# Kernel tuning notes

Measured on AMD Instinct MI355X. Metric: run time of the kernel, lower is better.

## Reference

```python
import jax, jax.numpy as jnp
import numpy as np

H = 8
DQ = 32
DK = 32
DV = 32
DC = DQ + DK  # concat dim for additive attention


def setup_inputs() -> dict:
    key = jax.random.key(0)
    ks = jax.random.split(key, 8)
    bs, Lq, Lk = 2, 384, 384
    q = jax.random.normal(ks[0], (bs, Lq, H * DQ), jnp.float32)
    k = jax.random.normal(ks[1], (bs, Lk, H * DK), jnp.float32)
    v = jax.random.normal(ks[2], (bs, Lk, H * DV), jnp.float32)
    q_sequence_lengths = jax.random.randint(ks[3], (bs,), 1, Lq + 1, dtype=jnp.int32)
    k_sequence_lengths = jax.random.randint(ks[4], (bs,), 1, Lk + 1, dtype=jnp.int32)
    bound = 1.0 / np.sqrt(DC)
    w1 = jax.random.uniform(ks[5], (H, DC, DC), jnp.float32, -bound, bound)
    b1 = jax.random.uniform(ks[6], (H, DC), jnp.float32, -bound, bound)
    w2 = jax.random.uniform(ks[7], (H, DC), jnp.float32, -1.0, 1.0)
    return {"q": q, "k": k, "v": v,
            "q_sequence_lengths": q_sequence_lengths,
            "k_sequence_lengths": k_sequence_lengths,
            "w1": w1, "b1": b1, "w2": w2}


def reference(q, k, v, q_sequence_lengths, k_sequence_lengths, w1, b1, w2):
    bs, Lq, _ = q.shape
    Lk = k.shape[1]
    # split heads: (b, h, L, d)
    qh = q.reshape(bs, Lq, H, DQ).transpose(0, 2, 1, 3)
    kh = k.reshape(bs, Lk, H, DK).transpose(0, 2, 1, 3)
    vh = v.reshape(bs, Lk, H, DV).transpose(0, 2, 1, 3)
    # additive scores: tanh(cat(q_i, k_j) @ W1 + b1) @ w2
    # cat @ W1 == q @ W1[:DQ] + k @ W1[DQ:]  (avoids materializing the cat)
    qW = jnp.einsum('bhqd,hde->bhqe', qh, w1[:, :DQ, :])
    kW = jnp.einsum('bhkd,hde->bhke', kh, w1[:, DQ:, :])
    hid = jnp.tanh(qW[:, :, :, None, :] + kW[:, :, None, :, :] + b1[None, :, None, None, :])  # (b,h,q,k,DC)
    scores = jnp.einsum('bhqke,he->bhqk', hid, w2)
    # key-side length mask (end padded)
    kmask = jnp.arange(Lk)[None, :] < k_sequence_lengths[:, None]  # (b, Lk)
    scores = jnp.where(kmask[:, None, None, :], scores, jnp.float32(-1e9))
    att = jax.nn.softmax(scores, axis=-1)  # (b,h,q,k)
    out = jnp.einsum('bhqk,bhkd->bqhd', att, vh)  # (b,q,h,DV)
    # query-side length mask zeros out padded query rows
    qmask = jnp.arange(Lq)[None, :] < q_sequence_lengths[:, None]  # (b, Lq)
    out = out * qmask[:, :, None, None].astype(out.dtype)
    return out.reshape(bs, Lq, H * DV), att
```

## Files before the change

### kernel.cpp

```cpp
#include <hip/hip_runtime.h>

#define NH 8
#define LQ 384
#define LK 384
#define BS 2

__global__ __launch_bounds__(256) void pre_ek_kernel(
    const float* __restrict__ kin, const float* __restrict__ w1,
    const float* __restrict__ b1, float* __restrict__ ws)
{
    __shared__ float tile[32][65];
    const int bid = blockIdx.x;
    const int bh = bid / 12, kt = bid % 12;
    const int b = bh >> 3, h = bh & 7;
    const int k0 = kt * 32;
    const int lane = threadIdx.x & 63, w = threadIdx.x >> 6;

    float w1c[32];
    const float* w1p = w1 + (size_t)(h * 64 + 32) * 64 + lane;
    #pragma unroll
    for (int d = 0; d < 32; ++d) w1c[d] = w1p[d * 64];
    const float bv = b1[h * 64 + lane];

    #pragma unroll
    for (int s = 0; s < 8; ++s) {
        int kr = w * 8 + s;
        const float* krow = kin + ((size_t)(b * LK + k0 + kr)) * (NH * 32) + h * 32;
        float acc = bv;
        #pragma unroll
        for (int d = 0; d < 32; ++d) acc = __builtin_fmaf(krow[d], w1c[d], acc);
        tile[kr][lane] = __expf(acc + acc);
    }
    __syncthreads();
    #pragma unroll
    for (int r = 0; r < 2; ++r) {
        int f = threadIdx.x + r * 256;
        int e4 = f >> 5, k32 = f & 31;
        float4 o;
        o.x = tile[k32][e4 * 4 + 0];
        o.y = tile[k32][e4 * 4 + 1];
        o.z = tile[k32][e4 * 4 + 2];
        o.w = tile[k32][e4 * 4 + 3];
        ((float4*)ws)[((size_t)(bh * 16 + e4)) * LK + k0 + k32] = o;
    }
}

__global__ __launch_bounds__(256) void attn_kernel(
    const float* __restrict__ qin, const float* __restrict__ vin,
    const int* __restrict__ qlens, const int* __restrict__ klens,
    const float* __restrict__ w1, const float* __restrict__ w2g,
    const float* __restrict__ ws,
    float* __restrict__ outg, float* __restrict__ attg)
{
    __shared__ __align__(16) float att_s[8][LK];
    __shared__ __align__(16) float eqs[8 * 64];
    __shared__ __align__(16) float w2s[4][64];

    const int tid = threadIdx.x, wave = tid >> 6, lane = tid & 63;
    const int bh = blockIdx.x / 48, tile = blockIdx.x % 48;
    const int b = bh >> 3, h = bh & 7;
    const int q0 = tile * 8;
    const int klen = klens[b], qlen = qlens[b];
    const int r0 = wave * 2;

    {
        const float* w1p = w1 + (size_t)h * 64 * 64 + lane;
        const float* q0p = qin + ((size_t)(b * LQ + q0 + r0)) * (NH * 32) + h * 32;
        const float* q1p = q0p + (NH * 32);
        float a0 = 0.f, a1 = 0.f;
        #pragma unroll
        for (int d = 0; d < 32; ++d) {
            float wv = w1p[d * 64];
            a0 = __builtin_fmaf(q0p[d], wv, a0);
            a1 = __builtin_fmaf(q1p[d], wv, a1);
        }
        eqs[(r0 + 0) * 64 + lane] = __expf(a0 + a0);
        eqs[(r0 + 1) * 64 + lane] = __expf(a1 + a1);
        w2s[wave][lane] = w2g[h * 64 + lane];
    }

    float sc0[6] = {0.f,0.f,0.f,0.f,0.f,0.f};
    float sc1[6] = {0.f,0.f,0.f,0.f,0.f,0.f};
    const float4* ekq  = (const float4*)ws + ((size_t)bh * 16) * LK + lane;
    const float4* eq0p = (const float4*)(eqs + (r0 + 0) * 64);
    const float4* eq1p = (const float4*)(eqs + (r0 + 1) * 64);
    const float4* w2p  = (const float4*)(&w2s[wave][0]);

    #pragma unroll 4
    for (int e4 = 0; e4 < 16; ++e4) {
        float4 e0 = eq0p[e4];
        float4 e1 = eq1p[e4];
        float4 wv = w2p[e4];
        const float4* kp = ekq + e4 * LK;
        #pragma unroll
        for (int c = 0; c < 6; ++c) {
            float4 kv = kp[c * 64];
            {
                float t0 = __builtin_fmaf(e0.x, kv.x, 1.f);
                float t1 = __builtin_fmaf(e0.y, kv.y, 1.f);
                float t2 = __builtin_fmaf(e0.z, kv.z, 1.f);
                float t3 = __builtin_fmaf(e0.w, kv.w, 1.f);
                float p12 = t0 * t1, p34 = t2 * t3;
                float n12 = wv.x * t1; n12 = __builtin_fmaf(wv.y, t0, n12);
                float n34 = wv.z * t3; n34 = __builtin_fmaf(wv.w, t2, n34);
                float num = n12 * p34; num = __builtin_fmaf(n34, p12, num);
                sc0[c] = __builtin_fmaf(num, __builtin_amdgcn_rcpf(p12 * p34), sc0[c]);
            }
            {
                float t0 = __builtin_fmaf(e1.x, kv.x, 1.f);
                float t1 = __builtin_fmaf(e1.y, kv.y, 1.f);
                float t2 = __builtin_fmaf(e1.z, kv.z, 1.f);
                float t3 = __builtin_fmaf(e1.w, kv.w, 1.f);
                float p12 = t0 * t1, p34 = t2 * t3;
                float n12 = wv.x * t1; n12 = __builtin_fmaf(wv.y, t0, n12);
                float n34 = wv.z * t3; n34 = __builtin_fmaf(wv.w, t2, n34);
                float num = n12 * p34; num = __builtin_fmaf(n34, p12, num);
                sc1[c] = __builtin_fmaf(num, __builtin_amdgcn_rcpf(p12 * p34), sc1[c]);
            }
        }
    }

    #pragma unroll
    for (int i = 0; i < 2; ++i) {
        const float* scp = i ? sc1 : sc0;
        int q = q0 + r0 + i;
        float s_[6], p[6];
        float m = -3.4e38f;
        #pragma unroll
        for (int j = 0; j < 6; ++j) {
            int kk = j * 64 + lane;
            float v = -2.0f * scp[j];
            s_[j] = (kk < klen) ? v : -3.4e38f;
            m = fmaxf(m, s_[j]);
        }
        #pragma unroll
        for (int off = 32; off >= 1; off >>= 1) m = fmaxf(m, __shfl_xor(m, off));
        float ssum = 0.f;
        #pragma unroll
        for (int j = 0; j < 6; ++j) {
            int kk = j * 64 + lane;
            p[j] = (kk < klen) ? __expf(s_[j] - m) : 0.f;
            ssum += p[j];
        }
        #pragma unroll
        for (int off = 32; off >= 1; off >>= 1) ssum += __shfl_xor(ssum, off);
        float inv = __builtin_amdgcn_rcpf(ssum);
        float* arow = att_s[r0 + i];
        float* ag = attg + ((size_t)(bh * LQ + q)) * LK;
        #pragma unroll
        for (int j = 0; j < 6; ++j) {
            float a = p[j] * inv;
            arow[j * 64 + lane] = a;
            ag[j * 64 + lane]   = a;
        }
    }

    const int kf = lane >> 3, dg = lane & 7;
    const float* vrow = vin + (size_t)b * LK * (NH * 32) + h * 32 + kf * (NH * 32) + dg * 4;
    const float* a0p = att_s[r0 + 0];
    const float* a1p = att_s[r0 + 1];
    float oa[2][4] = {{0.f,0.f,0.f,0.f},{0.f,0.f,0.f,0.f}};
    #pragma unroll 8
    for (int k0 = 0; k0 < LK; k0 += 8) {
        float4 vv = *(const float4*)(vrow + (size_t)k0 * (NH * 32));
        float a0 = a0p[k0 + kf];
        float a1 = a1p[k0 + kf];
        oa[0][0] = __builtin_fmaf(a0, vv.x, oa[0][0]);
        oa[0][1] = __builtin_fmaf(a0, vv.y, oa[0][1]);
        oa[0][2] = __builtin_fmaf(a0, vv.z, oa[0][2]);
        oa[0][3] = __builtin_fmaf(a0, vv.w, oa[0][3]);
        oa[1][0] = __builtin_fmaf(a1, vv.x, oa[1][0]);
        oa[1][1] = __builtin_fmaf(a1, vv.y, oa[1][1]);
        oa[1][2] = __builtin_fmaf(a1, vv.z, oa[1][2]);
        oa[1][3] = __builtin_fmaf(a1, vv.w, oa[1][3]);
    }
    #pragma unroll
    for (int i = 0; i < 2; ++i)
        #pragma unroll
        for (int u = 0; u < 4; ++u) {
            float x = oa[i][u];
            x += __shfl_xor(x, 8);
            x += __shfl_xor(x, 16);
            x += __shfl_xor(x, 32);
            oa[i][u] = x;
        }
    if (kf == 0) {
        #pragma unroll
        for (int i = 0; i < 2; ++i) {
            int q = q0 + r0 + i;
            float4 o4;
            o4.x = (q < qlen) ? oa[i][0] : 0.f;
            o4.y = (q < qlen) ? oa[i][1] : 0.f;
            o4.z = (q < qlen) ? oa[i][2] : 0.f;
            o4.w = (q < qlen) ? oa[i][3] : 0.f;
            ((float4*)(outg + ((size_t)(b * LQ + q)) * (NH * 32) + h * 32))[dg] = o4;
        }
    }
}

extern "C" void kernel_launch(void* const* d_in, const int* in_sizes, int n_in,
                              void* d_out, int out_size, void* d_ws, size_t ws_size,
                              hipStream_t stream) {
    const float* q    = (const float*)d_in[0];
    const float* k    = (const float*)d_in[1];
    const float* v    = (const float*)d_in[2];
    const int*   qlen = (const int*)d_in[3];
    const int*   klen = (const int*)d_in[4];
    const float* w1   = (const float*)d_in[5];
    const float* b1   = (const float*)d_in[6];
    const float* w2   = (const float*)d_in[7];
    float* out = (float*)d_out;
    float* att = out + (size_t)BS * LQ * NH * 32;
    float* ws  = (float*)d_ws;

    pre_ek_kernel<<<192, 256, 0, stream>>>(k, w1, b1, ws);
    attn_kernel<<<768, 256, 0, stream>>>(q, v, qlen, klen, w1, w2, ws, out, att);
}
```

Before: 105.1 us.

## Split key range across wave pairs with cross-wave softmax and PV reduction

Each block now handles 4 queries instead of 8. Pairs of waves split the 384 keys in halves, and the row max, row sum and PV partials are combined through shared memory with block barriers. The grid doubles to 1536 blocks and the per-thread score registers drop from 12 to 6. The key-side exp loads are also software-prefetched one e4 step ahead. This is meant to raise occupancy and parallelism, at the cost of extra __syncthreads, more exp(K) traffic per query, and redundant q projection work across more blocks.

```diff
diff --git a/kernel.cpp b/kernel.cpp
--- a/kernel.cpp
+++ b/kernel.cpp
@@ -52,54 +52,61 @@
     const float* __restrict__ ws,
     float* __restrict__ outg, float* __restrict__ attg)
 {
-    __shared__ __align__(16) float att_s[8][LK];
-    __shared__ __align__(16) float eqs[8 * 64];
-    __shared__ __align__(16) float w2s[4][64];
+    __shared__ __align__(16) float eqs[4 * 64];
+    __shared__ __align__(16) float att_h[4][2 * 192];
+    __shared__ __align__(16) float w2s[64];
+    __shared__ float smx[2][2][2];
+    __shared__ float ssm[2][2][2];
+    __shared__ __align__(16) float4 pvp[2][2][2][8];
 
     const int tid = threadIdx.x, wave = tid >> 6, lane = tid & 63;
-    const int bh = blockIdx.x / 48, tile = blockIdx.x % 48;
+    const int pair = wave >> 1, hh = wave & 1;
+    const int bh = blockIdx.x / 96, tile = blockIdx.x % 96;
     const int b = bh >> 3, h = bh & 7;
-    const int q0 = tile * 8;
+    const int q0 = tile * 4;
     const int klen = klens[b], qlen = qlens[b];
-    const int r0 = wave * 2;
 
     {
         const float* w1p = w1 + (size_t)h * 64 * 64 + lane;
-        const float* q0p = qin + ((size_t)(b * LQ + q0 + r0)) * (NH * 32) + h * 32;
-        const float* q1p = q0p + (NH * 32);
-        float a0 = 0.f, a1 = 0.f;
-        #pragma unroll
-        for (int d = 0; d < 32; ++d) {
-            float wv = w1p[d * 64];
-            a0 = __builtin_fmaf(q0p[d], wv, a0);
-            a1 = __builtin_fmaf(q1p[d], wv, a1);
-        }
-        eqs[(r0 + 0) * 64 + lane] = __expf(a0 + a0);
-        eqs[(r0 + 1) * 64 + lane] = __expf(a1 + a1);
-        w2s[wave][lane] = w2g[h * 64 + lane];
-    }
-
-    float sc0[6] = {0.f,0.f,0.f,0.f,0.f,0.f};
-    float sc1[6] = {0.f,0.f,0.f,0.f,0.f,0.f};
-    const float4* ekq  = (const float4*)ws + ((size_t)bh * 16) * LK + lane;
-    const float4* eq0p = (const float4*)(eqs + (r0 + 0) * 64);
-    const float4* eq1p = (const float4*)(eqs + (r0 + 1) * 64);
-    const float4* w2p  = (const float4*)(&w2s[wave][0]);
-
-    #pragma unroll 4
+        const float* qp  = qin + ((size_t)(b * LQ + q0 + wave)) * (NH * 32) + h * 32;
+        float a = 0.f;
+        #pragma unroll
+        for (int d = 0; d < 32; ++d) a = __builtin_fmaf(qp[d], w1p[d * 64], a);
+        eqs[wave * 64 + lane] = __expf(a + a);
+        if (wave == 0) w2s[lane] = w2g[h * 64 + lane];
+    }
+    __syncthreads();
+
+    float sc0[3] = {0.f, 0.f, 0.f};
+    float sc1[3] = {0.f, 0.f, 0.f};
+    const float4* ekq  = (const float4*)ws + ((size_t)bh * 16) * LK + hh * 192 + lane;
+    const float4* eq0p = (const float4*)(eqs + (2 * pair) * 64);
+    const float4* eq1p = (const float4*)(eqs + (2 * pair + 1) * 64);
+    const float4* w2p  = (const float4*)w2s;
+
+    float4 kv[3];
+    #pragma unroll
+    for (int c = 0; c < 3; ++c) kv[c] = ekq[c * 64];
+
+    #pragma unroll
     for (int e4 = 0; e4 < 16; ++e4) {
+        float4 nkv[3];
+        if (e4 < 15) {
+            const float4* np = ekq + (size_t)(e4 + 1) * LK;
+            #pragma unroll
+            for (int c = 0; c < 3; ++c) nkv[c] = np[c * 64];
+        }
         float4 e0 = eq0p[e4];
         float4 e1 = eq1p[e4];
         float4 wv = w2p[e4];
-        const float4* kp = ekq + e4 * LK;
-        #pragma unroll
-        for (int c = 0; c < 6; ++c) {
-            float4 kv = kp[c * 64];
+        #pragma unroll
+        for (int c = 0; c < 3; ++c) {
+            float4 kq = kv[c];
             {
-                float t0 = __builtin_fmaf(e0.x, kv.x, 1.f);
-                float t1 = __builtin_fmaf(e0.y, kv.y, 1.f);
-                float t2 = __builtin_fmaf(e0.z, kv.z, 1.f);
-                float t3 = __builtin_fmaf(e0.w, kv.w, 1.f);
+                float t0 = __builtin_fmaf(e0.x, kq.x, 1.f);
+                float t1 = __builtin_fmaf(e0.y, kq.y, 1.f);
+                float t2 = __builtin_fmaf(e0.z, kq.z, 1.f);
+                float t3 = __builtin_fmaf(e0.w, kq.w, 1.f);
                 float p12 = t0 * t1, p34 = t2 * t3;
                 float n12 = wv.x * t1; n12 = __builtin_fmaf(wv.y, t0, n12);
                 float n34 = wv.z * t3; n34 = __builtin_fmaf(wv.w, t2, n34);
@@ -107,10 +114,10 @@
                 sc0[c] = __builtin_fmaf(num, __builtin_amdgcn_rcpf(p12 * p34), sc0[c]);
             }
             {
-                float t0 = __builtin_fmaf(e1.x, kv.x, 1.f);
-                float t1 = __builtin_fmaf(e1.y, kv.y, 1.f);
-                float t2 = __builtin_fmaf(e1.z, kv.z, 1.f);
-                float t3 = __builtin_fmaf(e1.w, kv.w, 1.f);
+                float t0 = __builtin_fmaf(e1.x, kq.x, 1.f);
+                float t1 = __builtin_fmaf(e1.y, kq.y, 1.f);
+                float t2 = __builtin_fmaf(e1.z, kq.z, 1.f);
+                float t3 = __builtin_fmaf(e1.w, kq.w, 1.f);
                 float p12 = t0 * t1, p34 = t2 * t3;
                 float n12 = wv.x * t1; n12 = __builtin_fmaf(wv.y, t0, n12);
                 float n34 = wv.z * t3; n34 = __builtin_fmaf(wv.w, t2, n34);
@@ -118,83 +125,116 @@
                 sc1[c] = __builtin_fmaf(num, __builtin_amdgcn_rcpf(p12 * p34), sc1[c]);
             }
         }
-    }
-
-    #pragma unroll
-    for (int i = 0; i < 2; ++i) {
-        const float* scp = i ? sc1 : sc0;
-        int q = q0 + r0 + i;
-        float s_[6], p[6];
-        float m = -3.4e38f;
-        #pragma unroll
-        for (int j = 0; j < 6; ++j) {
-            int kk = j * 64 + lane;
-            float v = -2.0f * scp[j];
-            s_[j] = (kk < klen) ? v : -3.4e38f;
-            m = fmaxf(m, s_[j]);
-        }
-        #pragma unroll
-        for (int off = 32; off >= 1; off >>= 1) m = fmaxf(m, __shfl_xor(m, off));
-        float ssum = 0.f;
-        #pragma unroll
-        for (int j = 0; j < 6; ++j) {
-            int kk = j * 64 + lane;
-            p[j] = (kk < klen) ? __expf(s_[j] - m) : 0.f;
-            ssum += p[j];
-        }
-        #pragma unroll
-        for (int off = 32; off >= 1; off >>= 1) ssum += __shfl_xor(ssum, off);
-        float inv = __builtin_amdgcn_rcpf(ssum);
-        float* arow = att_s[r0 + i];
-        float* ag = attg + ((size_t)(bh * LQ + q)) * LK;
-        #pragma unroll
-        for (int j = 0; j < 6; ++j) {
-            float a = p[j] * inv;
-            arow[j * 64 + lane] = a;
-            ag[j * 64 + lane]   = a;
+        if (e4 < 15) {
+            #pragma unroll
+            for (int c = 0; c < 3; ++c) kv[c] = nkv[c];
+        }
+    }
+
+    float s0_[3], s1_[3];
+    float m0 = -3.4e38f, m1 = -3.4e38f;
+    #pragma unroll
+    for (int c = 0; c < 3; ++c) {
+        int kk = hh * 192 + c * 64 + lane;
+        s0_[c] = (kk < klen) ? -2.0f * sc0[c] : -3.4e38f;
+        s1_[c] = (kk < klen) ? -2.0f * sc1[c] : -3.4e38f;
+        m0 = fmaxf(m0, s0_[c]);
+        m1 = fmaxf(m1, s1_[c]);
+    }
+    #pragma unroll
+    for (int off = 32; off >= 1; off >>= 1) {
+        m0 = fmaxf(m0, __shfl_xor(m0, off));
+        m1 = fmaxf(m1, __shfl_xor(m1, off));
+    }
+    if (lane == 0) { smx[pair][0][hh] = m0; smx[pair][1][hh] = m1; }
+    __syncthreads();
+    m0 = fmaxf(smx[pair][0][0], smx[pair][0][1]);
+    m1 = fmaxf(smx[pair][1][0], smx[pair][1][1]);
+
+    float p0[3], p1[3];
+    float u0 = 0.f, u1 = 0.f;
+    #pragma unroll
+    for (int c = 0; c < 3; ++c) {
+        int kk = hh * 192 + c * 64 + lane;
+        p0[c] = (kk < klen) ? __expf(s0_[c] - m0) : 0.f;
+        p1[c] = (kk < klen) ? __expf(s1_[c] - m1) : 0.f;
+        u0 += p0[c];
+        u1 += p1[c];
+    }
+    #pragma unroll
+    for (int off = 32; off >= 1; off >>= 1) {
+        u0 += __shfl_xor(u0, off);
+        u1 += __shfl_xor(u1, off);
+    }
+    if (lane == 0) { ssm[pair][0][hh] = u0; ssm[pair][1][hh] = u1; }
+    __syncthreads();
+    float inv0 = __builtin_amdgcn_rcpf(ssm[pair][0][0] + ssm[pair][0][1]);
+    float inv1 = __builtin_amdgcn_rcpf(ssm[pair][1][0] + ssm[pair][1][1]);
+
+    {
+        float* ar = att_h[wave];
+        #pragma unroll
+        for (int c = 0; c < 3; ++c) {
+            ar[c * 64 + lane]       = p0[c] * inv0;
+            ar[192 + c * 64 + lane] = p1[c] * inv1;
         }
     }
 
     const int kf = lane >> 3, dg = lane & 7;
-    const float* vrow = vin + (size_t)b * LK * (NH * 32) + h * 32 + kf * (NH * 32) + dg * 4;
-    const float* a0p = att_s[r0 + 0];
-    const float* a1p = att_s[r0 + 1];
-    float oa[2][4] = {{0.f,0.f,0.f,0.f},{0.f,0.f,0.f,0.f}};
+    const float* vbase = vin + (size_t)b * LK * (NH * 32) + h * 32
+                       + (size_t)(hh * 192 + kf) * (NH * 32) + dg * 4;
+    const float* a0p = att_h[wave];
+    const float* a1p = att_h[wave] + 192;
+    float oa0[4] = {0.f,0.f,0.f,0.f}, oa1[4] = {0.f,0.f,0.f,0.f};
     #pragma unroll 8
-    for (int k0 = 0; k0 < LK; k0 += 8) {
-        float4 vv = *(const float4*)(vrow + (size_t)k0 * (NH * 32));
+    for (int k0 = 0; k0 < 192; k0 += 8) {
+        float4 vv = *(const float4*)(vbase + (size_t)k0 * (NH * 32));
         float a0 = a0p[k0 + kf];
         float a1 = a1p[k0 + kf];
-        oa[0][0] = __builtin_fmaf(a0, vv.x, oa[0][0]);
-        oa[0][1] = __builtin_fmaf(a0, vv.y, oa[0][1]);
-        oa[0][2] = __builtin_fmaf(a0, vv.z, oa[0][2]);
-        oa[0][3] = __builtin_fmaf(a0, vv.w, oa[0][3]);
-        oa[1][0] = __builtin_fmaf(a1, vv.x, oa[1][0]);
-        oa[1][1] = __builtin_fmaf(a1, vv.y, oa[1][1]);
-        oa[1][2] = __builtin_fmaf(a1, vv.z, oa[1][2]);
-        oa[1][3] = __builtin_fmaf(a1, vv.w, oa[1][3]);
-    }
-    #pragma unroll
-    for (int i = 0; i < 2; ++i)
-        #pragma unroll
-        for (int u = 0; u < 4; ++u) {
-            float x = oa[i][u];
-            x += __shfl_xor(x, 8);
-            x += __shfl_xor(x, 16);
-            x += __shfl_xor(x, 32);
-            oa[i][u] = x;
-        }
+        oa0[0] = __builtin_fmaf(a0, vv.x, oa0[0]);
+        oa0[1] = __builtin_fmaf(a0, vv.y, oa0[1]);
+        oa0[2] = __builtin_fmaf(a0, vv.z, oa0[2]);
+        oa0[3] = __builtin_fmaf(a0, vv.w, oa0[3]);
+        oa1[0] = __builtin_fmaf(a1, vv.x, oa1[0]);
+        oa1[1] = __builtin_fmaf(a1, vv.y, oa1[1]);
+        oa1[2] = __builtin_fmaf(a1, vv.z, oa1[2]);
+        oa1[3] = __builtin_fmaf(a1, vv.w, oa1[3]);
+    }
+    #pragma unroll
+    for (int u = 0; u < 4; ++u) {
+        oa0[u] += __shfl_xor(oa0[u], 8);
+        oa0[u] += __shfl_xor(oa0[u], 16);
+        oa0[u] += __shfl_xor(oa0[u], 32);
+        oa1[u] += __shfl_xor(oa1[u], 8);
+        oa1[u] += __shfl_xor(oa1[u], 16);
+        oa1[u] += __shfl_xor(oa1[u], 32);
+    }
     if (kf == 0) {
-        #pragma unroll
-        for (int i = 0; i < 2; ++i) {
-            int q = q0 + r0 + i;
-            float4 o4;
-            o4.x = (q < qlen) ? oa[i][0] : 0.f;
-            o4.y = (q < qlen) ? oa[i][1] : 0.f;
-            o4.z = (q < qlen) ? oa[i][2] : 0.f;
-            o4.w = (q < qlen) ? oa[i][3] : 0.f;
-            ((float4*)(outg + ((size_t)(b * LQ + q)) * (NH * 32) + h * 32))[dg] = o4;
-        }
+        pvp[pair][hh][0][dg] = make_float4(oa0[0], oa0[1], oa0[2], oa0[3]);
+        pvp[pair][hh][1][dg] = make_float4(oa1[0], oa1[1], oa1[2], oa1[3]);
+    }
+    __syncthreads();
+
+    if (lane < 8) {
+        int q = q0 + wave;
+        float4 xa = pvp[wave >> 1][0][wave & 1][lane];
+        float4 xb = pvp[wave >> 1][1][wave & 1][lane];
+        float4 o4;
+        bool ok = (q < qlen);
+        o4.x = ok ? (xa.x + xb.x) : 0.f;
+        o4.y = ok ? (xa.y + xb.y) : 0.f;
+        o4.z = ok ? (xa.z + xb.z) : 0.f;
+        o4.w = ok ? (xa.w + xb.w) : 0.f;
+        ((float4*)(outg + ((size_t)(b * LQ + q)) * (NH * 32) + h * 32))[lane] = o4;
+    }
+
+    {
+        float* ag = attg + ((size_t)(bh * LQ + q0 + 2 * pair)) * LK + hh * 192;
+        #pragma unroll
+        for (int c = 0; c < 3; ++c) ag[c * 64 + lane] = p0[c] * inv0;
+        ag += LK;
+        #pragma unroll
+        for (int c = 0; c < 3; ++c) ag[c * 64 + lane] = p1[c] * inv1;
     }
 }
 
@@ -214,5 +254,5 @@
     float* ws  = (float*)d_ws;
 
     pre_ek_kernel<<<192, 256, 0, stream>>>(k, w1, b1, ws);
-    attn_kernel<<<768, 256, 0, stream>>>(q, v, qlen, klen, w1, w2, ws, out, att);
+    attn_kernel<<<1536, 256, 0, stream>>>(q, v, qlen, klen, w1, w2, ws, out, att);
 }
```

New measurement: 100.8 us. 4.1% less time.
